# Kernel optimization log

Hardware: AMD Instinct MI355X
Metric: run time of the kernel (lower is better)

The kernel has to match this reference:

```python
import jax, jax.numpy as jnp
import numpy as np

H, D = 4, 64          # n_heads, feats_per_head (hidden_size = H*D = 256)
NEG_SLOPE = 0.2       # DGL GATv2Conv default negative_slope

N_GT, N_UBS, N_AG = 100000, 20000, 20000
E_SEEN, E_NEAR = 320000, 160000
F_GT, F_UBS, F_AG = 8, 8, 16
HID = H * D


def _linear_params(key, fan_in, fan_out):
    kw, kb = jax.random.split(key)
    s = 1.0 / np.sqrt(fan_in)
    W = jax.random.uniform(kw, (fan_in, fan_out), jnp.float32, -s, s)
    b = jax.random.uniform(kb, (fan_out,), jnp.float32, -s, s)
    return W, b


def setup_inputs() -> dict:
    key = jax.random.key(0)
    ks = jax.random.split(key, 16)
    inp = {
        'x_gt': jax.random.normal(ks[0], (N_GT, F_GT), jnp.float32),
        'x_ubs': jax.random.normal(ks[1], (N_UBS, F_UBS), jnp.float32),
        'x_agent': jax.random.normal(ks[2], (N_AG, F_AG), jnp.float32),
        'seen_src': jax.random.randint(ks[3], (E_SEEN,), 0, N_GT, jnp.int32),
        'seen_dst': jax.random.randint(ks[4], (E_SEEN,), 0, N_AG, jnp.int32),
        'near_src': jax.random.randint(ks[5], (E_NEAR,), 0, N_UBS, jnp.int32),
        'near_dst': jax.random.randint(ks[6], (E_NEAR,), 0, N_AG, jnp.int32),
    }
    # GATv2Conv 'seen': (gt -> agent)
    inp['Ws_seen'], inp['bs_seen'] = _linear_params(ks[7], F_GT, HID)
    inp['Wd_seen'], inp['bd_seen'] = _linear_params(ks[8], F_AG, HID)
    inp['attn_seen'] = jax.random.normal(ks[9], (H, D), jnp.float32) * 0.1
    inp['Wr_seen'], inp['br_seen'] = _linear_params(ks[10], F_AG, HID)
    # GATv2Conv 'near': (ubs -> agent)
    inp['Ws_near'], inp['bs_near'] = _linear_params(ks[11], F_UBS, HID)
    inp['Wd_near'], inp['bd_near'] = _linear_params(ks[12], F_AG, HID)
    inp['attn_near'] = jax.random.normal(ks[13], (H, D), jnp.float32) * 0.1
    inp['Wr_near'], inp['br_near'] = _linear_params(ks[14], F_AG, HID)
    # aggregation MLP: Linear(2*HID, HID) + ReLU
    inp['W_aggr'], inp['b_aggr'] = _linear_params(ks[15], 2 * HID, HID)
    return inp


def _gatv2(h_src, h_dst, src, dst, Ws, bs, Wd, bd, attn, Wr, br, n_dst):
    # DGL GATv2Conv, bipartite, residual=True, allow_zero_in_degree, ReLU activation
    fs = (h_src @ Ws + bs).reshape(-1, H, D)   # [Ns,H,D]
    fd = (h_dst @ Wd + bd).reshape(-1, H, D)   # [Nd,H,D]
    e = jax.nn.leaky_relu(fs[src] + fd[dst], NEG_SLOPE)     # [E,H,D]
    scores = jnp.einsum('ehd,hd->eh', e, attn)              # [E,H]
    # edge softmax over incoming edges of each dst node
    m = jax.ops.segment_max(scores, dst, num_segments=n_dst)
    m = jnp.where(jnp.isfinite(m), m, 0.0)                  # zero-in-degree guard
    ex = jnp.exp(scores - m[dst])
    denom = jax.ops.segment_sum(ex, dst, num_segments=n_dst)
    alpha = ex / denom[dst]                                 # [E,H]
    rst = jax.ops.segment_sum(alpha[:, :, None] * fs[src], dst, num_segments=n_dst)
    rst = rst + (h_dst @ Wr + br).reshape(-1, H, D)         # residual
    return jax.nn.relu(rst).reshape(n_dst, H * D)


def reference(x_gt, x_ubs, x_agent, seen_src, seen_dst, near_src, near_dst,
              Ws_seen, bs_seen, Wd_seen, bd_seen, attn_seen, Wr_seen, br_seen,
              Ws_near, bs_near, Wd_near, bd_near, attn_near, Wr_near, br_near,
              W_aggr, b_aggr):
    n_ag = x_agent.shape[0]
    x1 = _gatv2(x_gt, x_agent, seen_src, seen_dst,
                Ws_seen, bs_seen, Wd_seen, bd_seen, attn_seen, Wr_seen, br_seen, n_ag)
    x2 = _gatv2(x_ubs, x_agent, near_src, near_dst,
                Ws_near, bs_near, Wd_near, bd_near, attn_near, Wr_near, br_near, n_ag)
    x_out = jnp.concatenate((x1, x2), axis=1)               # [N_ag, 2*HID]
    return jax.nn.relu(x_out @ W_aggr + b_aggr)             # [N_ag, HID]
```

## Files before the change

kernel.cpp:

```cpp
#include <hip/hip_runtime.h>
#include <math.h>

#define NEG 0.2f
#define LDSW 520
#define CAP 48

typedef short bf16x8 __attribute__((ext_vector_type(8)));
typedef float f32x4  __attribute__((ext_vector_type(4)));
typedef float f32x2  __attribute__((ext_vector_type(2)));

static __device__ __forceinline__ f32x2 pkfma(f32x2 a, f32x2 b, f32x2 c) {
    return __builtin_elementwise_fma(a, b, c);
}
static __device__ __forceinline__ f32x2 splat2(float x) { return (f32x2){x, x}; }

static __device__ __forceinline__ unsigned short f2bf(float f) {
    unsigned int x = __float_as_uint(f);
    unsigned int r = (x + 0x7FFFu + ((x >> 16) & 1u)) >> 16;
    return (unsigned short)r;
}
static __device__ __forceinline__ float rlane(float v, int l) {
    return __int_as_float(__builtin_amdgcn_readlane(__float_as_int(v), l));
}

#define DPP_ADD(x, ctrl) \
    ((x) + __int_as_float(__builtin_amdgcn_update_dpp( \
        __float_as_int(x), __float_as_int(x), (ctrl), 0xF, 0xF, true)))
static __device__ __forceinline__ float rowsum16(float v) {
    v = DPP_ADD(v, 0xB1);
    v = DPP_ADD(v, 0x4E);
    v = DPP_ADD(v, 0x141);
    v = DPP_ADD(v, 0x140);
    return v;
}

__global__ void k_hist_scatter(
    const int* __restrict__ src_s, const int* __restrict__ dst_s, int Es,
    const int* __restrict__ src_n, const int* __restrict__ dst_n, int En,
    int* __restrict__ deg_s, int* __restrict__ deg_n,
    int* __restrict__ csr_s, int* __restrict__ csr_n,
    const float* __restrict__ W, unsigned short* __restrict__ Wt)
{
    int i = blockIdx.x * 256 + threadIdx.x;
    if (i < Es) {
        int d = dst_s[i];
        int p = atomicAdd(&deg_s[d], 1);
        if (p < CAP) csr_s[d * CAP + p] = src_s[i];
    }
    int j = i - Es;
    if (j >= 0 && j < En) {
        int d = dst_n[j];
        int p = atomicAdd(&deg_n[d], 1);
        if (p < CAP) csr_n[d * CAP + p] = src_n[j];
    }
    if (i < 512 * 256) {
        int k = i >> 8, n = i & 255;
        Wt[(size_t)n * 512 + k] = f2bf(W[i]);
    }
}

#define EDGE_BODY { \
    f32x2 x0 = splat2(rlane(r0, j * 8 + 0)); \
    f32x2 x1 = splat2(rlane(r0, j * 8 + 1)); \
    f32x2 x2 = splat2(rlane(r0, j * 8 + 2)); \
    f32x2 x3 = splat2(rlane(r0, j * 8 + 3)); \
    f32x2 x4 = splat2(rlane(r0, j * 8 + 4)); \
    f32x2 x5 = splat2(rlane(r0, j * 8 + 5)); \
    f32x2 x6 = splat2(rlane(r0, j * 8 + 6)); \
    f32x2 x7 = splat2(rlane(r0, j * 8 + 7)); \
    f32x2 fs01 = bs01, fs23 = bs23; \
    fs01 = pkfma(x0, ws01[0], fs01); fs23 = pkfma(x0, ws23[0], fs23); \
    fs01 = pkfma(x1, ws01[1], fs01); fs23 = pkfma(x1, ws23[1], fs23); \
    fs01 = pkfma(x2, ws01[2], fs01); fs23 = pkfma(x2, ws23[2], fs23); \
    fs01 = pkfma(x3, ws01[3], fs01); fs23 = pkfma(x3, ws23[3], fs23); \
    fs01 = pkfma(x4, ws01[4], fs01); fs23 = pkfma(x4, ws23[4], fs23); \
    fs01 = pkfma(x5, ws01[5], fs01); fs23 = pkfma(x5, ws23[5], fs23); \
    fs01 = pkfma(x6, ws01[6], fs01); fs23 = pkfma(x6, ws23[6], fs23); \
    fs01 = pkfma(x7, ws01[7], fs01); fs23 = pkfma(x7, ws23[7], fs23); \
    f32x2 t01 = fs01 + fd01r; \
    f32x2 t23 = fs23 + fd23r; \
    t01 = __builtin_elementwise_max(t01, NEG * t01); \
    t23 = __builtin_elementwise_max(t23, NEG * t23); \
    f32x2 scp = t01 * at01; \
    scp = pkfma(t23, at23, scp); \
    float sc = scp.x + scp.y; \
    sc = rowsum16(sc); \
    float p = __expf(sc);    \
    l += p; \
    f32x2 pp = splat2(p); \
    a01 = pkfma(pp, fs01, a01); \
    a23 = pkfma(pp, fs23, a23); }

static __device__ __forceinline__ void gat_layer4(
    const float* __restrict__ x_src, const int* __restrict__ csr,
    const float* __restrict__ Ws, const float* __restrict__ bs,
    const float* __restrict__ Wd, const float* __restrict__ bd,
    const float* __restrict__ at,
    const float* __restrict__ Wr, const float* __restrict__ br,
    float xag, int lane, int w4, int nb, int n_dst,
    const int* st, const int* dg,
    const int* i1pre, const float* x0pre,
    unsigned short* __restrict__ ldsbase)
{
    const int d0 = lane * 4;
    const int gs = lane >> 3;
    const int w8 = lane & 7;

    f32x2 fd01[4], fd23[4], fr01[4], fr23[4];
    {
        float4 bdv = *(const float4*)&bd[d0];
        float4 brv = *(const float4*)&br[d0];
#pragma unroll
        for (int j = 0; j < 4; ++j) {
            fd01[j] = (f32x2){bdv.x, bdv.y}; fd23[j] = (f32x2){bdv.z, bdv.w};
            fr01[j] = (f32x2){brv.x, brv.y}; fr23[j] = (f32x2){brv.z, brv.w};
        }
#pragma unroll
        for (int k = 0; k < 16; ++k) {
            float4 wd = *(const float4*)&Wd[k * 256 + d0];
            float4 wr = *(const float4*)&Wr[k * 256 + d0];
            f32x2 wd01 = {wd.x, wd.y}, wd23 = {wd.z, wd.w};
            f32x2 wr01 = {wr.x, wr.y}, wr23 = {wr.z, wr.w};
#pragma unroll
            for (int j = 0; j < 4; ++j) {
                f32x2 xk = splat2(rlane(xag, j * 16 + k));
                fd01[j] = pkfma(xk, wd01, fd01[j]);
                fd23[j] = pkfma(xk, wd23, fd23[j]);
                fr01[j] = pkfma(xk, wr01, fr01[j]);
                fr23[j] = pkfma(xk, wr23, fr23[j]);
            }
        }
    }

    f32x2 ws01[8], ws23[8];
#pragma unroll
    for (int k = 0; k < 8; ++k) {
        float4 w = *(const float4*)&Ws[k * 256 + d0];
        ws01[k] = (f32x2){w.x, w.y};
        ws23[k] = (f32x2){w.z, w.w};
    }
    f32x2 bs01, bs23, at01, at23;
    {
        float4 b4 = *(const float4*)&bs[d0];
        float4 a4 = *(const float4*)&at[d0];
        bs01 = (f32x2){b4.x, b4.y}; bs23 = (f32x2){b4.z, b4.w};
        at01 = (f32x2){a4.x, a4.y}; at23 = (f32x2){a4.z, a4.w};
    }

#pragma unroll
    for (int rep = 0; rep < 4; ++rep) {
        const int node = nb + rep * 4 + w4;
        if (node >= n_dst) continue;

        const int start = st[rep];
        const int deg   = dg[rep];
        const f32x2 fd01r = fd01[rep], fd23r = fd23[rep];

        float l = 0.f;
        f32x2 a01 = {0.f, 0.f}, a23 = {0.f, 0.f};

        if (deg > 0) {
            float r0 = x0pre[rep];
            int   i1 = i1pre[rep];
            const int nfull = deg >> 3, tail = deg & 7;

            for (int c = 0; c < nfull; ++c) {
                float r1 = x_src[(size_t)i1 * 8 + w8];
                int e2 = c * 8 + 16 + gs; e2 = (e2 < deg) ? e2 : deg - 1;
                int i2 = csr[start + e2];
#pragma unroll
                for (int j = 0; j < 8; ++j) EDGE_BODY
                r0 = r1; i1 = i2;
            }
            if (tail) {
#pragma unroll
                for (int j = 0; j < 8; ++j)
                    if (j < tail) EDGE_BODY
            }
        }

        float inv = (l > 0.f) ? 1.f / l : 0.f;
        ushort4 o;
        o.x = f2bf(fmaxf(fmaf(a01.x, inv, fr01[rep].x), 0.f));
        o.y = f2bf(fmaxf(fmaf(a01.y, inv, fr01[rep].y), 0.f));
        o.z = f2bf(fmaxf(fmaf(a23.x, inv, fr23[rep].x), 0.f));
        o.w = f2bf(fmaxf(fmaf(a23.y, inv, fr23[rep].y), 0.f));
        *(ushort4*)(ldsbase + (rep * 4 + w4) * LDSW) = o;
    }
}

__global__ __launch_bounds__(512) void k_gatmlp(
    const float* __restrict__ xsrc_s, const int* __restrict__ deg_s_a, const int* __restrict__ csr_s,
    const float* __restrict__ Ws_s, const float* __restrict__ bs_s,
    const float* __restrict__ Wd_s, const float* __restrict__ bd_s,
    const float* __restrict__ at_s,
    const float* __restrict__ Wr_s, const float* __restrict__ br_s,
    const float* __restrict__ xsrc_n, const int* __restrict__ deg_n_a, const int* __restrict__ csr_n,
    const float* __restrict__ Ws_n, const float* __restrict__ bs_n,
    const float* __restrict__ Wd_n, const float* __restrict__ bd_n,
    const float* __restrict__ at_n,
    const float* __restrict__ Wr_n, const float* __restrict__ br_n,
    const float* __restrict__ x_ag,
    const unsigned short* __restrict__ Wt, const float* __restrict__ bmlp,
    float* __restrict__ out, int n_dst)
{
    __shared__ unsigned short xt[16 * LDSW];

    const int t = threadIdx.x;
    const int wave = t >> 6, lane = t & 63;
    const int w4 = wave & 3;
    const bool seen = wave < 4;
    const int gs = lane >> 3, w8 = lane & 7;
    const int nb = (int)blockIdx.x * 16;

    const float* x_src = seen ? xsrc_s : xsrc_n;
    const int*   degp  = seen ? deg_s_a : deg_n_a;
    const int*   csr   = seen ? csr_s  : csr_n;
    const float* Ws    = seen ? Ws_s   : Ws_n;
    const float* bs    = seen ? bs_s   : bs_n;
    const float* Wd    = seen ? Wd_s   : Wd_n;
    const float* bd    = seen ? bd_s   : bd_n;
    const float* at    = seen ? at_s   : at_n;
    const float* Wr    = seen ? Wr_s   : Wr_n;
    const float* br    = seen ? br_s   : br_n;
    const int col = seen ? 0 : 256;

    int gnode = nb + ((lane >> 4) << 2) + w4;
    int gn = (gnode < n_dst) ? gnode : (n_dst - 1);
    float xag = x_ag[(size_t)gn * 16 + (lane & 15)];

    int st[4], dg[4];
#pragma unroll
    for (int j = 0; j < 4; ++j) {
        int nd = nb + j * 4 + w4;
        nd = (nd < n_dst) ? nd : (n_dst - 1);
        int d = degp[nd];
        dg[j] = (d < CAP) ? d : CAP;
        st[j] = nd * CAP;
    }

    int i0[4], i1[4];
#pragma unroll
    for (int j = 0; j < 4; ++j) {
        int dgj = dg[j];
        if (dgj > 0) {
            int e0 = (gs < dgj) ? gs : dgj - 1;
            int e1 = (8 + gs < dgj) ? 8 + gs : dgj - 1;
            i0[j] = csr[st[j] + e0];
            i1[j] = csr[st[j] + e1];
        } else { i0[j] = 0; i1[j] = 0; }
    }
    float x0[4];
#pragma unroll
    for (int j = 0; j < 4; ++j)
        x0[j] = x_src[(size_t)i0[j] * 8 + w8];

    if (seen) __builtin_amdgcn_s_setprio(1);
    gat_layer4(x_src, csr, Ws, bs, Wd, bd, at, Wr, br,
               xag, lane, w4, nb, n_dst, st, dg, i1, x0, &xt[col + lane * 4]);
    __builtin_amdgcn_s_setprio(0);

    __syncthreads();

    const int m16 = lane & 15, q = lane >> 4;
    const unsigned short* w0 = Wt + (size_t)(wave * 32 + m16) * 512 + q * 8;
    const unsigned short* w1 = w0 + 16 * 512;
    const unsigned short* ap = &xt[m16 * LDSW + q * 8];

    f32x4 ac0 = {0.f, 0.f, 0.f, 0.f}, ac1 = ac0;
#pragma unroll
    for (int k0 = 0; k0 < 512; k0 += 32) {
        bf16x8 a  = *(const bf16x8*)(ap + k0);
        bf16x8 b0 = *(const bf16x8*)(w0 + k0);
        bf16x8 b1 = *(const bf16x8*)(w1 + k0);
        ac0 = __builtin_amdgcn_mfma_f32_16x16x32_bf16(a, b0, ac0, 0, 0, 0);
        ac1 = __builtin_amdgcn_mfma_f32_16x16x32_bf16(a, b1, ac1, 0, 0, 0);
    }

#define EPI(AC, J) { \
        int coln = wave * 32 + (J) * 16 + m16; \
        float bv = bmlp[coln]; \
        _Pragma("unroll") \
        for (int r = 0; r < 4; ++r) { \
            int orow = nb + q * 4 + r; \
            if (orow < n_dst) \
                out[(size_t)orow * 256 + coln] = fmaxf(AC[r] + bv, 0.f); \
        } }
    EPI(ac0, 0) EPI(ac1, 1)
#undef EPI
}

extern "C" void kernel_launch(void* const* d_in, const int* in_sizes, int n_in,
                              void* d_out, int out_size, void* d_ws, size_t ws_size,
                              hipStream_t stream) {
    const float* x_gt   = (const float*)d_in[0];
    const float* x_ubs  = (const float*)d_in[1];
    const float* x_ag   = (const float*)d_in[2];
    const int* seen_src = (const int*)d_in[3];
    const int* seen_dst = (const int*)d_in[4];
    const int* near_src = (const int*)d_in[5];
    const int* near_dst = (const int*)d_in[6];
    const float* Ws_s = (const float*)d_in[7];  const float* bs_s = (const float*)d_in[8];
    const float* Wd_s = (const float*)d_in[9];  const float* bd_s = (const float*)d_in[10];
    const float* at_s = (const float*)d_in[11];
    const float* Wr_s = (const float*)d_in[12]; const float* br_s = (const float*)d_in[13];
    const float* Ws_n = (const float*)d_in[14]; const float* bs_n = (const float*)d_in[15];
    const float* Wd_n = (const float*)d_in[16]; const float* bd_n = (const float*)d_in[17];
    const float* at_n = (const float*)d_in[18];
    const float* Wr_n = (const float*)d_in[19]; const float* br_n = (const float*)d_in[20];
    const float* W_a  = (const float*)d_in[21]; const float* b_a  = (const float*)d_in[22];

    const int n_ag = in_sizes[2] / 16;
    const int E_s  = in_sizes[3];
    const int E_n  = in_sizes[5];

    char* ws = (char*)d_ws;
    int* deg_s = (int*)ws;              ws += (size_t)n_ag * 4;
    int* deg_n = (int*)ws;              ws += (size_t)n_ag * 4;
    int* csr_s = (int*)ws;              ws += (size_t)n_ag * CAP * 4;
    int* csr_n = (int*)ws;              ws += (size_t)n_ag * CAP * 4;
    unsigned short* Wt = (unsigned short*)ws;

    hipMemsetAsync(deg_s, 0, (size_t)n_ag * 8, stream);

    int gE = (E_s + E_n + 255) / 256;
    k_hist_scatter<<<gE, 256, 0, stream>>>(
        seen_src, seen_dst, E_s, near_src, near_dst, E_n,
        deg_s, deg_n, csr_s, csr_n, W_a, Wt);

    int gN = (n_ag + 15) / 16;
    k_gatmlp<<<gN, 512, 0, stream>>>(
        x_gt,  deg_s, csr_s, Ws_s, bs_s, Wd_s, bd_s, at_s, Wr_s, br_s,
        x_ubs, deg_n, csr_n, Ws_n, bs_n, Wd_n, bd_n, at_n, Wr_n, br_n,
        x_ag, Wt, b_a, (float*)d_out, n_ag);
}
```

Before: 255.9 us.

## Rebalance waves: 5 seen waves x3 nodes, 3 near waves x5 nodes per block

Each block now handles 15 destination nodes instead of 16. Five waves process the 'seen' relation with 3 nodes each and three waves process the 'near' relation with 5 nodes each, replacing the even 4/4 split. Seen edges are twice as many as near edges, so this is meant to even out per-wave edge work and shorten the slowest wave before the block barrier. In exchange the MFMA tile wastes one padding row, which is zeroed in LDS and masked on store. The grid grows slightly, and the near waves carry more registers because of the 5-node unroll.

```diff
diff --git a/kernel.cpp b/kernel.cpp
--- a/kernel.cpp
+++ b/kernel.cpp
@@ -91,27 +91,53 @@
     a01 = pkfma(pp, fs01, a01); \
     a23 = pkfma(pp, fs23, a23); }
 
-static __device__ __forceinline__ void gat_layer4(
-    const float* __restrict__ x_src, const int* __restrict__ csr,
+template<int NREP>
+static __device__ __forceinline__ void gat_layerN(
+    const float* __restrict__ x_src, const int* __restrict__ degp,
+    const int* __restrict__ csr,
     const float* __restrict__ Ws, const float* __restrict__ bs,
     const float* __restrict__ Wd, const float* __restrict__ bd,
     const float* __restrict__ at,
     const float* __restrict__ Wr, const float* __restrict__ br,
-    float xag, int lane, int w4, int nb, int n_dst,
-    const int* st, const int* dg,
-    const int* i1pre, const float* x0pre,
-    unsigned short* __restrict__ ldsbase)
+    float xag, float xag2, int lane, int nodebase, int ldsrow, int n_dst,
+    unsigned short* __restrict__ xt, int col)
 {
     const int d0 = lane * 4;
     const int gs = lane >> 3;
     const int w8 = lane & 7;
 
-    f32x2 fd01[4], fd23[4], fr01[4], fr23[4];
+    int st[NREP], dg[NREP];
+#pragma unroll
+    for (int j = 0; j < NREP; ++j) {
+        int nd = nodebase + j;
+        nd = (nd < n_dst) ? nd : (n_dst - 1);
+        int d = degp[nd];
+        dg[j] = (d < CAP) ? d : CAP;
+        st[j] = nd * CAP;
+    }
+
+    int i0[NREP], i1[NREP];
+#pragma unroll
+    for (int j = 0; j < NREP; ++j) {
+        int dgj = dg[j];
+        if (dgj > 0) {
+            int e0 = (gs < dgj) ? gs : dgj - 1;
+            int e1 = (8 + gs < dgj) ? 8 + gs : dgj - 1;
+            i0[j] = csr[st[j] + e0];
+            i1[j] = csr[st[j] + e1];
+        } else { i0[j] = 0; i1[j] = 0; }
+    }
+    float x0[NREP];
+#pragma unroll
+    for (int j = 0; j < NREP; ++j)
+        x0[j] = x_src[(size_t)i0[j] * 8 + w8];
+
+    f32x2 fd01[NREP], fd23[NREP], fr01[NREP], fr23[NREP];
     {
         float4 bdv = *(const float4*)&bd[d0];
         float4 brv = *(const float4*)&br[d0];
 #pragma unroll
-        for (int j = 0; j < 4; ++j) {
+        for (int j = 0; j < NREP; ++j) {
             fd01[j] = (f32x2){bdv.x, bdv.y}; fd23[j] = (f32x2){bdv.z, bdv.w};
             fr01[j] = (f32x2){brv.x, brv.y}; fr23[j] = (f32x2){brv.z, brv.w};
         }
@@ -122,12 +148,13 @@
             f32x2 wd01 = {wd.x, wd.y}, wd23 = {wd.z, wd.w};
             f32x2 wr01 = {wr.x, wr.y}, wr23 = {wr.z, wr.w};
 #pragma unroll
-            for (int j = 0; j < 4; ++j) {
-                f32x2 xk = splat2(rlane(xag, j * 16 + k));
-                fd01[j] = pkfma(xk, wd01, fd01[j]);
-                fd23[j] = pkfma(xk, wd23, fd23[j]);
-                fr01[j] = pkfma(xk, wr01, fr01[j]);
-                fr23[j] = pkfma(xk, wr23, fr23[j]);
+            for (int j = 0; j < NREP; ++j) {
+                float xk = (j < 4) ? rlane(xag, j * 16 + k) : rlane(xag2, k);
+                f32x2 xkk = splat2(xk);
+                fd01[j] = pkfma(xkk, wd01, fd01[j]);
+                fd23[j] = pkfma(xkk, wd23, fd23[j]);
+                fr01[j] = pkfma(xkk, wr01, fr01[j]);
+                fr23[j] = pkfma(xkk, wr23, fr23[j]);
             }
         }
     }
@@ -148,8 +175,8 @@
     }
 
 #pragma unroll
-    for (int rep = 0; rep < 4; ++rep) {
-        const int node = nb + rep * 4 + w4;
+    for (int rep = 0; rep < NREP; ++rep) {
+        const int node = nodebase + rep;
         if (node >= n_dst) continue;
 
         const int start = st[rep];
@@ -160,17 +187,17 @@
         f32x2 a01 = {0.f, 0.f}, a23 = {0.f, 0.f};
 
         if (deg > 0) {
-            float r0 = x0pre[rep];
-            int   i1 = i1pre[rep];
+            float r0 = x0[rep];
+            int   i1c = i1[rep];
             const int nfull = deg >> 3, tail = deg & 7;
 
             for (int c = 0; c < nfull; ++c) {
-                float r1 = x_src[(size_t)i1 * 8 + w8];
+                float r1 = x_src[(size_t)i1c * 8 + w8];
                 int e2 = c * 8 + 16 + gs; e2 = (e2 < deg) ? e2 : deg - 1;
                 int i2 = csr[start + e2];
 #pragma unroll
                 for (int j = 0; j < 8; ++j) EDGE_BODY
-                r0 = r1; i1 = i2;
+                r0 = r1; i1c = i2;
             }
             if (tail) {
 #pragma unroll
@@ -185,7 +212,7 @@
         o.y = f2bf(fmaxf(fmaf(a01.y, inv, fr01[rep].y), 0.f));
         o.z = f2bf(fmaxf(fmaf(a23.x, inv, fr23[rep].x), 0.f));
         o.w = f2bf(fmaxf(fmaf(a23.y, inv, fr23[rep].y), 0.f));
-        *(ushort4*)(ldsbase + (rep * 4 + w4) * LDSW) = o;
+        *(ushort4*)(&xt[(ldsrow + rep) * LDSW + col + d0]) = o;
     }
 }
 
@@ -208,10 +235,10 @@
 
     const int t = threadIdx.x;
     const int wave = t >> 6, lane = t & 63;
-    const int w4 = wave & 3;
-    const bool seen = wave < 4;
-    const int gs = lane >> 3, w8 = lane & 7;
-    const int nb = (int)blockIdx.x * 16;
+    const bool seen = wave < 5;
+    const int nb = (int)blockIdx.x * 15;
+
+    if (t < 256) ((unsigned int*)&xt[15 * LDSW])[t] = 0u;
 
     const float* x_src = seen ? xsrc_s : xsrc_n;
     const int*   degp  = seen ? deg_s_a : deg_n_a;
@@ -225,40 +252,26 @@
     const float* br    = seen ? br_s   : br_n;
     const int col = seen ? 0 : 256;
 
-    int gnode = nb + ((lane >> 4) << 2) + w4;
-    int gn = (gnode < n_dst) ? gnode : (n_dst - 1);
-    float xag = x_ag[(size_t)gn * 16 + (lane & 15)];
-
-    int st[4], dg[4];
-#pragma unroll
-    for (int j = 0; j < 4; ++j) {
-        int nd = nb + j * 4 + w4;
-        nd = (nd < n_dst) ? nd : (n_dst - 1);
-        int d = degp[nd];
-        dg[j] = (d < CAP) ? d : CAP;
-        st[j] = nd * CAP;
-    }
-
-    int i0[4], i1[4];
-#pragma unroll
-    for (int j = 0; j < 4; ++j) {
-        int dgj = dg[j];
-        if (dgj > 0) {
-            int e0 = (gs < dgj) ? gs : dgj - 1;
-            int e1 = (8 + gs < dgj) ? 8 + gs : dgj - 1;
-            i0[j] = csr[st[j] + e0];
-            i1[j] = csr[st[j] + e1];
-        } else { i0[j] = 0; i1[j] = 0; }
-    }
-    float x0[4];
-#pragma unroll
-    for (int j = 0; j < 4; ++j)
-        x0[j] = x_src[(size_t)i0[j] * 8 + w8];
-
-    if (seen) __builtin_amdgcn_s_setprio(1);
-    gat_layer4(x_src, csr, Ws, bs, Wd, bd, at, Wr, br,
-               xag, lane, w4, nb, n_dst, st, dg, i1, x0, &xt[col + lane * 4]);
-    __builtin_amdgcn_s_setprio(0);
+    const int nodebase = seen ? (nb + wave * 3) : (nb + (wave - 5) * 5);
+    const int ldsrow   = nodebase - nb;
+
+    const int nrep = seen ? 3 : 5;
+    int slot = lane >> 4; slot = (slot < nrep) ? slot : nrep - 1;
+    int gnode = nodebase + slot;
+    gnode = (gnode < n_dst) ? gnode : (n_dst - 1);
+    float xag = x_ag[(size_t)gnode * 16 + (lane & 15)];
+    float xag2 = 0.f;
+    if (!seen) {
+        int g2 = nodebase + 4; g2 = (g2 < n_dst) ? g2 : (n_dst - 1);
+        xag2 = x_ag[(size_t)g2 * 16 + (lane & 15)];
+    }
+
+    if (seen)
+        gat_layerN<3>(x_src, degp, csr, Ws, bs, Wd, bd, at, Wr, br,
+                      xag, xag2, lane, nodebase, ldsrow, n_dst, xt, col);
+    else
+        gat_layerN<5>(x_src, degp, csr, Ws, bs, Wd, bd, at, Wr, br,
+                      xag, xag2, lane, nodebase, ldsrow, n_dst, xt, col);
 
     __syncthreads();
 
@@ -282,8 +295,9 @@
         float bv = bmlp[coln]; \
         _Pragma("unroll") \
         for (int r = 0; r < 4; ++r) { \
-            int orow = nb + q * 4 + r; \
-            if (orow < n_dst) \
+            int lrow = q * 4 + r; \
+            int orow = nb + lrow; \
+            if (lrow < 15 && orow < n_dst) \
                 out[(size_t)orow * 256 + coln] = fmaxf(AC[r] + bv, 0.f); \
         } }
     EPI(ac0, 0) EPI(ac1, 1)
@@ -328,7 +342,7 @@
         seen_src, seen_dst, E_s, near_src, near_dst, E_n,
         deg_s, deg_n, csr_s, csr_n, W_a, Wt);
 
-    int gN = (n_ag + 15) / 16;
+    int gN = (n_ag + 14) / 15;
     k_gatmlp<<<gN, 512, 0, stream>>>(
         x_gt,  deg_s, csr_s, Ws_s, bs_s, Wd_s, bd_s, at_s, Wr_s, br_s,
         x_ubs, deg_n, csr_n, Ws_n, bs_n, Wd_n, bd_n, at_n, Wr_n, br_n,
```

Result: slower. 271.0 us (+5.9%).
